# Kernel tuning notes

Measured on AMD Instinct MI355X. Metric: run time of the kernel, lower is better.

The kernel has to match this reference:

```python
import jax, jax.numpy as jnp
import numpy as np

B, S, H = 1, 2048, 4608
NH, NKV, HD = 36, 4, 128
GROUP = NH // NKV  # 9
ROPE_THETA = 100000.0
SLIDING_WINDOW = 1024


def _rope_tables(seq_len, head_dim):
    inv_freq = 1.0 / (ROPE_THETA ** (jnp.arange(0, head_dim, 2, dtype=jnp.float32) / head_dim))
    ang = jnp.arange(seq_len, dtype=jnp.float32)[:, None] * inv_freq[None, :]  # [S, HD/2]
    emb = jnp.concatenate([ang, ang], axis=-1)  # [S, HD]
    return jnp.cos(emb), jnp.sin(emb)


def setup_inputs() -> dict:
    key = jax.random.key(0)
    ks = jax.random.split(key, 10)
    std = 0.02
    cos_table, sin_table = _rope_tables(S, HD)
    return {
        "hidden_states": jax.random.normal(ks[0], (B, S, H), jnp.float32),
        "position_ids": jnp.broadcast_to(jnp.arange(S, dtype=jnp.int64)[None, :], (B, S)),
        "cos_table": cos_table,
        "sin_table": sin_table,
        "q_w": jax.random.normal(ks[1], (NH * HD, H), jnp.float32) * std,
        "q_b": jax.random.normal(ks[2], (NH * HD,), jnp.float32) * std,
        "k_w": jax.random.normal(ks[3], (NKV * HD, H), jnp.float32) * std,
        "k_b": jax.random.normal(ks[4], (NKV * HD,), jnp.float32) * std,
        "v_w": jax.random.normal(ks[5], (NKV * HD, H), jnp.float32) * std,
        "v_b": jax.random.normal(ks[6], (NKV * HD,), jnp.float32) * std,
        "o_w": jax.random.normal(ks[7], (H, NH * HD), jnp.float32) * std,
        "o_b": jax.random.normal(ks[8], (H,), jnp.float32) * std,
        "sliding_window": SLIDING_WINDOW,
    }


def _rotate_half(x):
    x1, x2 = jnp.split(x, 2, axis=-1)
    return jnp.concatenate([-x2, x1], axis=-1)


def reference(hidden_states, position_ids, cos_table, sin_table,
              q_w, q_b, k_w, k_b, v_w, v_b, o_w, o_b, sliding_window):
    bsz, q_len, _ = hidden_states.shape
    scaling = HD ** -0.5

    q = (hidden_states @ q_w.T + q_b).reshape(bsz, q_len, NH, HD)
    k = (hidden_states @ k_w.T + k_b).reshape(bsz, q_len, NKV, HD)
    v = (hidden_states @ v_w.T + v_b).reshape(bsz, q_len, NKV, HD)

    # RoPE with explicit cos/sin, unsqueeze_dim=2 ('bsnd' layout)
    cos = cos_table[position_ids][:, :, None, :]  # [B, S, 1, HD]
    sin = sin_table[position_ids][:, :, None, :]
    q = q * cos + _rotate_half(q) * sin
    k = k * cos + _rotate_half(k) * sin

    # GQA: group Q heads per KV head
    qg = q.reshape(bsz, q_len, NKV, GROUP, HD)
    logits = jnp.einsum('bqgrd,bkgd->bgrqk', qg, k) * scaling  # [B, NKV, GROUP, S, S]

    # causal + sliding-window mask: attend where k <= q and q - k < window
    idx = jnp.arange(q_len)
    mask = (idx[:, None] >= idx[None, :]) & (idx[:, None] - idx[None, :] < sliding_window)
    logits = jnp.where(mask[None, None, None, :, :], logits, jnp.finfo(logits.dtype).min)

    probs = jax.nn.softmax(logits, axis=-1)
    attn = jnp.einsum('bgrqk,bkgd->bqgrd', probs, v).reshape(bsz, q_len, NH * HD)
    return attn @ o_w.T + o_b
```

## Files before the change

kernel.cpp:

```cpp
#include <hip/hip_runtime.h>
#include <stdint.h>

typedef __attribute__((ext_vector_type(8))) __bf16 bf16x8;
typedef __attribute__((ext_vector_type(4))) float f32x4;
typedef __attribute__((ext_vector_type(8))) unsigned short u16x8;
typedef __attribute__((ext_vector_type(4))) unsigned short u16x4;

#define SEQ 2048
#define HID 4608
#define NQKV 5632
#define NHEAD 36
#define NKVH 4
#define HDIM 128
#define WINDOW 1024

__device__ __forceinline__ unsigned short f2b(float f) {
    unsigned u = __builtin_bit_cast(unsigned, f);
    u += 0x7fffu + ((u >> 16) & 1u);
    return (unsigned short)(u >> 16);
}
__device__ __forceinline__ float b2f(unsigned short h) {
    unsigned u = ((unsigned)h) << 16;
    return __builtin_bit_cast(float, u);
}

#define GLD16(gp, lp) __builtin_amdgcn_global_load_lds( \
    (const __attribute__((address_space(1))) void*)(gp), \
    (__attribute__((address_space(3))) void*)(lp), 16, 0, 0)

#define VMCNT8() asm volatile("s_waitcnt vmcnt(8)" ::: "memory")
#define VMCNT4() asm volatile("s_waitcnt vmcnt(4)" ::: "memory")
#define VMCNT0() asm volatile("s_waitcnt vmcnt(0)" ::: "memory")
#define BARRIER() asm volatile("s_barrier" ::: "memory")

__global__ __launch_bounds__(256) void conv_kernel(const float* __restrict__ src,
                                                   unsigned short* __restrict__ dst, int n4) {
    int stride = gridDim.x * blockDim.x;
    for (int i = blockIdx.x * blockDim.x + threadIdx.x; i < n4; i += stride) {
        float4 v = ((const float4*)src)[i];
        ushort4 o;
        o.x = f2b(v.x); o.y = f2b(v.y); o.z = f2b(v.z); o.w = f2b(v.w);
        ((ushort4*)dst)[i] = o;
    }
}

__global__ __launch_bounds__(512, 2) void gemm256_kernel(
    const unsigned short* __restrict__ A,
    const unsigned short* __restrict__ W,
    void* __restrict__ out,
    const float* __restrict__ b0, const float* __restrict__ b1, const float* __restrict__ b2,
    int N, int K, int GX, int outf32)
{
    __shared__ alignas(16) unsigned short ldsA[2][256 * 64];
    __shared__ alignas(16) unsigned short ldsB[2][256 * 64];

    const int tid = threadIdx.x;
    const int w = tid >> 6, lane = tid & 63;
    const int r16 = lane & 15, kg = lane >> 4;
    const int wm = w >> 2, wn = w & 3;

    const int cpx = gridDim.x >> 3;
    const int o = blockIdx.x;
    const int id = (o & 7) * cpx + (o >> 3);
    const int bx = id % GX, by = id / GX;
    const int row0 = by * 256, col0 = bx * 256;

    const int lr = lane >> 3;
    const int lc = lane & 7;
    const int cg = lc ^ lr;
    const unsigned short* Abase = A + (size_t)row0 * K;
    const unsigned short* Wbase = W + (size_t)col0 * K;

    auto STG = [&](const unsigned short* Mat, unsigned short* ldsSlot, int hf, int kb) {
#pragma unroll
        for (int j = 0; j < 2; ++j) {
            int row = hf * 128 + (w * 2 + j) * 8 + lr;
            GLD16(Mat + (size_t)row * K + kb + cg * 8,
                  (char*)ldsSlot + hf * 16384 + (w * 2 + j) * 1024);
        }
    };

    const int NITER = K >> 7;
    f32x4 acc[8][4] = {};
    const int swz = r16 & 7;

    bf16x8 af[4][2], bfA[2][2], bfB[2][2];

#define DSR_A(mh, Sl) \
_Pragma("unroll") for (int mi = 0; mi < 4; ++mi) \
_Pragma("unroll") for (int kh = 0; kh < 2; ++kh) \
    af[mi][kh] = *(const bf16x8*)((Sl) + (wm * 128 + (mh) * 64 + mi * 16 + r16) * 64 + ((kh * 4 + kg) ^ swz) * 8);
#define DSR_B(nh, Sl, BF) \
_Pragma("unroll") for (int ni = 0; ni < 2; ++ni) \
_Pragma("unroll") for (int kh = 0; kh < 2; ++kh) \
    BF[ni][kh] = *(const bf16x8*)((Sl) + (wn * 64 + (nh) * 32 + ni * 16 + r16) * 64 + ((kh * 4 + kg) ^ swz) * 8);
#define MFMA_Q(mh, nh, BF) \
    asm volatile("s_waitcnt lgkmcnt(0)" ::: "memory"); \
    __builtin_amdgcn_sched_barrier(0); \
    __builtin_amdgcn_s_setprio(1); \
_Pragma("unroll") for (int mi = 0; mi < 4; ++mi) \
_Pragma("unroll") for (int ni = 0; ni < 2; ++ni) \
_Pragma("unroll") for (int kh = 0; kh < 2; ++kh) \
    acc[(mh) * 4 + mi][(nh) * 2 + ni] = __builtin_amdgcn_mfma_f32_16x16x32_bf16(af[mi][kh], BF[ni][kh], acc[(mh) * 4 + mi][(nh) * 2 + ni], 0, 0, 0); \
    __builtin_amdgcn_s_setprio(0); \
    __builtin_amdgcn_sched_barrier(0);

    STG(Abase, ldsA[0], 0, 0);  STG(Abase, ldsA[0], 1, 0);
    STG(Wbase, ldsB[0], 0, 0);  STG(Wbase, ldsB[0], 1, 0);
    STG(Abase, ldsA[1], 0, 64); STG(Abase, ldsA[1], 1, 64);
    STG(Wbase, ldsB[1], 0, 64); STG(Wbase, ldsB[1], 1, 64);
    VMCNT0();
    BARRIER();

    for (int i = 0; i < NITER; ++i) {
        const unsigned short* A0 = ldsA[0];
        const unsigned short* B0 = ldsB[0];
        const unsigned short* A1 = ldsA[1];
        const unsigned short* B1 = ldsB[1];
        const bool st = (i + 1 < NITER);
        const int kb0 = (i + 1) * 128;
        const int kb1 = kb0 + 64;

        DSR_A(0, A0); DSR_B(0, B0, bfA);
        BARRIER();
        MFMA_Q(0, 0, bfA);
        BARRIER();
        DSR_B(1, B0, bfB);
        BARRIER();
        MFMA_Q(0, 1, bfB);
        BARRIER();
        DSR_A(1, A0);
        if (st) STG(Wbase, ldsB[0], 0, kb0);
        BARRIER();
        MFMA_Q(1, 1, bfB);
        BARRIER();
        if (st) { STG(Abase, ldsA[0], 0, kb0); VMCNT4(); } else { VMCNT0(); }
        BARRIER();
        MFMA_Q(1, 0, bfA);
        BARRIER();
        DSR_A(0, A1); DSR_B(0, B1, bfA);
        if (st) STG(Abase, ldsA[0], 1, kb0);
        BARRIER();
        MFMA_Q(0, 0, bfA);
        BARRIER();
        DSR_B(1, B1, bfB);
        if (st) STG(Wbase, ldsB[0], 1, kb0);
        BARRIER();
        MFMA_Q(0, 1, bfB);
        BARRIER();
        DSR_A(1, A1);
        if (st) { STG(Wbase, ldsB[1], 0, kb1); STG(Wbase, ldsB[1], 1, kb1); }
        BARRIER();
        MFMA_Q(1, 1, bfB);
        BARRIER();
        if (st) { STG(Abase, ldsA[1], 0, kb1); STG(Abase, ldsA[1], 1, kb1); VMCNT8(); }
        BARRIER();
        MFMA_Q(1, 0, bfA);
        BARRIER();
    }

    if (!outf32) {
        unsigned short* O = (unsigned short*)out;
#pragma unroll
        for (int m = 0; m < 8; ++m)
#pragma unroll
            for (int n = 0; n < 4; ++n)
#pragma unroll
                for (int r = 0; r < 4; ++r) {
                    int row = row0 + wm * 128 + m * 16 + kg * 4 + r;
                    int col = col0 + wn * 64 + n * 16 + r16;
                    float bias = (col < HID) ? b0[col]
                               : (col < HID + 512 ? b1[col - HID] : b2[col - HID - 512]);
                    O[(size_t)row * N + col] = f2b(acc[m][n][r] + bias);
                }
    } else {
        float* O = (float*)out;
#pragma unroll
        for (int m = 0; m < 8; ++m)
#pragma unroll
            for (int n = 0; n < 4; ++n)
#pragma unroll
                for (int r = 0; r < 4; ++r) {
                    int row = row0 + wm * 128 + m * 16 + kg * 4 + r;
                    int col = col0 + wn * 64 + n * 16 + r16;
                    O[(size_t)row * N + col] = acc[m][n][r] + b0[col];
                }
    }
#undef DSR_A
#undef DSR_B
#undef MFMA_Q
}

__global__ __launch_bounds__(256) void rope_kernel(unsigned short* __restrict__ qkv,
                                                   const float* __restrict__ cos_t,
                                                   const float* __restrict__ sin_t) {
    int idx = blockIdx.x * 256 + threadIdx.x;
    int d = idx & 63;
    int t = idx >> 6;
    int head = t % 40;
    int s = t / 40;
    int base = head < NHEAD ? head * HDIM : HID + (head - NHEAD) * HDIM;
    size_t off = (size_t)s * NQKV + base;
    float x = b2f(qkv[off + d]);
    float y = b2f(qkv[off + d + 64]);
    float c = cos_t[s * HDIM + d];
    float sn = sin_t[s * HDIM + d];
    qkv[off + d]      = f2b(x * c - y * sn);
    qkv[off + d + 64] = f2b(y * c + x * sn);
}

__global__ __launch_bounds__(256) void vtrans_kernel(const unsigned short* __restrict__ qkv,
                                                     unsigned short* __restrict__ vtg) {
    __shared__ unsigned short tile[32][36];
    const int s0 = blockIdx.x * 32, d0 = blockIdx.y * 32, kvh = blockIdx.z;
    const int lid = threadIdx.x;
    {
        int sl = lid >> 3, dc = (lid & 7) * 4;
        u16x4 v = *(const u16x4*)(qkv + (size_t)(s0 + sl) * NQKV + HID + 512 + kvh * HDIM + d0 + dc);
#pragma unroll
        for (int i = 0; i < 4; ++i) tile[sl][dc + i] = v[i];
    }
    __syncthreads();
    {
        int dl = lid >> 3, sc = (lid & 7) * 4;
        u16x4 v;
#pragma unroll
        for (int i = 0; i < 4; ++i) v[i] = tile[sc + i][dl];
        *(u16x4*)(vtg + (size_t)kvh * HDIM * SEQ + (size_t)(d0 + dl) * SEQ + s0 + sc) = v;
    }
}

#define KSTR 136
#define VSTR 72
#define PSTR 88
__global__ __launch_bounds__(256) void attn_kernel(const unsigned short* __restrict__ qkv,
                                                   const unsigned short* __restrict__ vtg,
                                                   unsigned short* __restrict__ aout)
{
    __shared__ alignas(16) unsigned short Ks[64 * KSTR];
    __shared__ alignas(16) unsigned short Vt[128 * VSTR];
    __shared__ alignas(16) unsigned short Ps[4 * 16 * PSTR];
    const int h = blockIdx.x, qb = blockIdx.y;
    const int q0 = qb * 64;
    const int kvh = h / 9;
    const int tid = threadIdx.x, wid = tid >> 6, lane = tid & 63;
    const int r16 = lane & 15, kg = lane >> 4;
    const int qbase = q0 + wid * 16;
    const unsigned short* vsrc = vtg + (size_t)kvh * HDIM * SEQ;

    bf16x8 qf[4];
    {
        const unsigned short* qrow = qkv + (size_t)(qbase + r16) * NQKV + h * HDIM;
#pragma unroll
        for (int kk = 0; kk < 4; ++kk)
            qf[kk] = *(const bf16x8*)(qrow + kk * 32 + kg * 8);
    }

    f32x4 o[8] = {};
    float mrow[4], lrow[4];
#pragma unroll
    for (int r = 0; r < 4; ++r) { mrow[r] = -1e30f; lrow[r] = 0.f; }

    int lo = q0 - (WINDOW - 1); if (lo < 0) lo = 0; lo &= ~63;
    unsigned short* myP = Ps + wid * 16 * PSTR;
    const float scale = 0.08838834764831845f;

    for (int kt = lo; kt <= q0; kt += 64) {
        for (int c = tid; c < 1024; c += 256) {
            int key = c >> 4, dc = c & 15;
            const unsigned short* kp = qkv + (size_t)(kt + key) * NQKV + HID + kvh * HDIM + dc * 8;
            *(u16x8*)(Ks + key * KSTR + dc * 8) = *(const u16x8*)kp;
            int d = c >> 3, k8 = (c & 7) * 8;
            *(u16x8*)(Vt + d * VSTR + k8) = *(const u16x8*)(vsrc + (size_t)d * SEQ + kt + k8);
        }
        __syncthreads();

        f32x4 sc[4] = {};
#pragma unroll
        for (int t = 0; t < 4; ++t)
#pragma unroll
            for (int kk = 0; kk < 4; ++kk) {
                bf16x8 kf = *(const bf16x8*)(Ks + (t * 16 + r16) * KSTR + kk * 32 + kg * 8);
                sc[t] = __builtin_amdgcn_mfma_f32_16x16x32_bf16(qf[kk], kf, sc[t], 0, 0, 0);
            }

        float p[4][4], mt[4];
#pragma unroll
        for (int r = 0; r < 4; ++r) mt[r] = -1e30f;
#pragma unroll
        for (int t = 0; t < 4; ++t)
#pragma unroll
            for (int r = 0; r < 4; ++r) {
                int q = qbase + kg * 4 + r;
                int key = kt + t * 16 + r16;
                bool valid = (key <= q) && (q - key < WINDOW);
                float v = valid ? sc[t][r] * scale : -1e30f;
                p[t][r] = v;
                mt[r] = fmaxf(mt[r], v);
            }
#pragma unroll
        for (int mask = 1; mask <= 8; mask <<= 1)
#pragma unroll
            for (int r = 0; r < 4; ++r)
                mt[r] = fmaxf(mt[r], __shfl_xor(mt[r], mask, 64));

        float alpha[4], tsum[4];
#pragma unroll
        for (int r = 0; r < 4; ++r) {
            float mnew = fmaxf(mrow[r], mt[r]);
            alpha[r] = __expf(mrow[r] - mnew);
            mrow[r] = mnew;
            tsum[r] = 0.f;
        }
#pragma unroll
        for (int t = 0; t < 4; ++t)
#pragma unroll
            for (int r = 0; r < 4; ++r) {
                float e = __expf(p[t][r] - mrow[r]);
                p[t][r] = e;
                tsum[r] += e;
            }
#pragma unroll
        for (int mask = 1; mask <= 8; mask <<= 1)
#pragma unroll
            for (int r = 0; r < 4; ++r)
                tsum[r] += __shfl_xor(tsum[r], mask, 64);
#pragma unroll
        for (int r = 0; r < 4; ++r)
            lrow[r] = lrow[r] * alpha[r] + tsum[r];
#pragma unroll
        for (int n = 0; n < 8; ++n)
#pragma unroll
            for (int r = 0; r < 4; ++r)
                o[n][r] = o[n][r] * alpha[r];

#pragma unroll
        for (int t = 0; t < 4; ++t)
#pragma unroll
            for (int r = 0; r < 4; ++r)
                myP[(kg * 4 + r) * PSTR + t * 16 + r16] = f2b(p[t][r]);
        asm volatile("s_waitcnt lgkmcnt(0)" ::: "memory");

#pragma unroll
        for (int kc = 0; kc < 2; ++kc) {
            bf16x8 pa = *(const bf16x8*)(myP + r16 * PSTR + kc * 32 + kg * 8);
#pragma unroll
            for (int n = 0; n < 8; ++n) {
                bf16x8 vb = *(const bf16x8*)(Vt + (n * 16 + r16) * VSTR + kc * 32 + kg * 8);
                o[n] = __builtin_amdgcn_mfma_f32_16x16x32_bf16(pa, vb, o[n], 0, 0, 0);
            }
        }
        __syncthreads();
    }

#pragma unroll
    for (int n = 0; n < 8; ++n)
#pragma unroll
        for (int r = 0; r < 4; ++r) {
            int q = qbase + kg * 4 + r;
            aout[(size_t)q * HID + h * HDIM + n * 16 + r16] = f2b(o[n][r] / lrow[r]);
        }
}

extern "C" void kernel_launch(void* const* d_in, const int* in_sizes, int n_in,
                              void* d_out, int out_size, void* d_ws, size_t ws_size,
                              hipStream_t stream) {
    const float* hidden = (const float*)d_in[0];
    const float* cos_t = (const float*)d_in[2];
    const float* sin_t = (const float*)d_in[3];
    const float* q_w = (const float*)d_in[4];
    const float* q_b = (const float*)d_in[5];
    const float* k_w = (const float*)d_in[6];
    const float* k_b = (const float*)d_in[7];
    const float* v_w = (const float*)d_in[8];
    const float* v_b = (const float*)d_in[9];
    const float* o_w = (const float*)d_in[10];
    const float* o_b = (const float*)d_in[11];

    char* ws = (char*)d_ws;
    unsigned short* hbf  = (unsigned short*)ws;
    unsigned short* attn = hbf;
    unsigned short* wqkv = (unsigned short*)(ws + 18874368);
    unsigned short* vtg  = wqkv;
    unsigned short* wo   = (unsigned short*)(ws + 70778880);
    unsigned short* qkv  = (unsigned short*)(ws + 113246208);

    dim3 blk(256);
    conv_kernel<<<2048, blk, 0, stream>>>(hidden, hbf, (SEQ * HID) / 4);
    conv_kernel<<<2048, blk, 0, stream>>>(q_w, wqkv, (HID * HID) / 4);
    conv_kernel<<<2048, blk, 0, stream>>>(k_w, wqkv + (size_t)HID * HID, (512 * HID) / 4);
    conv_kernel<<<2048, blk, 0, stream>>>(v_w, wqkv + (size_t)5120 * HID, (512 * HID) / 4);
    conv_kernel<<<2048, blk, 0, stream>>>(o_w, wo, (HID * HID) / 4);

    gemm256_kernel<<<dim3(176), dim3(512), 0, stream>>>(hbf, wqkv, qkv, q_b, k_b, v_b, NQKV, HID, 22, 0);
    rope_kernel<<<(SEQ * 40 * 64) / 256, blk, 0, stream>>>(qkv, cos_t, sin_t);
    vtrans_kernel<<<dim3(SEQ / 32, HDIM / 32, NKVH), blk, 0, stream>>>(qkv, vtg);
    attn_kernel<<<dim3(NHEAD, SEQ / 64), blk, 0, stream>>>(qkv, vtg, attn);
    gemm256_kernel<<<dim3(144), dim3(512), 0, stream>>>(attn, wo, d_out, o_b, nullptr, nullptr, HID, HID, 18, 1);
}
```

Measured before the change: 438.8 us.

## Prefetch next K/V tile into registers in attention and merge conversion launches

The attention loop now loads the next 64-key K and V tiles into registers right after the barrier, so the global loads overlap with the QK and PV MFMA work of the current tile. It also replaces the trailing __syncthreads with a raw s_barrier. Separately, the five fp32-to-bf16 conversion launches are merged into one grid-stride kernel that picks source and destination by index range, cutting launch overhead. The prefetch raises register pressure through eight extra 16-byte vectors per thread, which may lower occupancy.

```diff
diff --git a/kernel.cpp b/kernel.cpp
--- a/kernel.cpp
+++ b/kernel.cpp
@@ -33,14 +33,26 @@
 #define VMCNT0() asm volatile("s_waitcnt vmcnt(0)" ::: "memory")
 #define BARRIER() asm volatile("s_barrier" ::: "memory")
 
-__global__ __launch_bounds__(256) void conv_kernel(const float* __restrict__ src,
-                                                   unsigned short* __restrict__ dst, int n4) {
+__global__ __launch_bounds__(256) void conv_all_kernel(
+    const float* __restrict__ s0, unsigned short* __restrict__ d0, int n0,
+    const float* __restrict__ s1, unsigned short* __restrict__ d1, int n1,
+    const float* __restrict__ s2, unsigned short* __restrict__ d2, int n2,
+    const float* __restrict__ s3, unsigned short* __restrict__ d3, int n3,
+    const float* __restrict__ s4, unsigned short* __restrict__ d4, int n4)
+{
+    int total = n0 + n1 + n2 + n3 + n4;
     int stride = gridDim.x * blockDim.x;
-    for (int i = blockIdx.x * blockDim.x + threadIdx.x; i < n4; i += stride) {
-        float4 v = ((const float4*)src)[i];
+    for (int i = blockIdx.x * blockDim.x + threadIdx.x; i < total; i += stride) {
+        const float* src; unsigned short* dst; int j = i;
+        if (j < n0) { src = s0; dst = d0; }
+        else if ((j -= n0) < n1) { src = s1; dst = d1; }
+        else if ((j -= n1) < n2) { src = s2; dst = d2; }
+        else if ((j -= n2) < n3) { src = s3; dst = d3; }
+        else { j -= n3; src = s4; dst = d4; }
+        float4 v = ((const float4*)src)[j];
         ushort4 o;
         o.x = f2b(v.x); o.y = f2b(v.y); o.z = f2b(v.z); o.w = f2b(v.w);
-        ((ushort4*)dst)[i] = o;
+        ((ushort4*)dst)[j] = o;
     }
 }
 
@@ -265,15 +277,30 @@
     unsigned short* myP = Ps + wid * 16 * PSTR;
     const float scale = 0.08838834764831845f;
 
+    u16x8 kreg[4], vreg[4];
+#define PREF(KT) \
+_Pragma("unroll") for (int j = 0; j < 4; ++j) { \
+        int c = tid + j * 256; \
+        int key = c >> 4, dc = c & 15; \
+        kreg[j] = *(const u16x8*)(qkv + (size_t)((KT) + key) * NQKV + HID + kvh * HDIM + dc * 8); \
+        int d = c >> 3, k8 = (c & 7) * 8; \
+        vreg[j] = *(const u16x8*)(vsrc + (size_t)d * SEQ + (KT) + k8); \
+    }
+
+    PREF(lo);
+
     for (int kt = lo; kt <= q0; kt += 64) {
-        for (int c = tid; c < 1024; c += 256) {
+#pragma unroll
+        for (int j = 0; j < 4; ++j) {
+            int c = tid + j * 256;
             int key = c >> 4, dc = c & 15;
-            const unsigned short* kp = qkv + (size_t)(kt + key) * NQKV + HID + kvh * HDIM + dc * 8;
-            *(u16x8*)(Ks + key * KSTR + dc * 8) = *(const u16x8*)kp;
+            *(u16x8*)(Ks + key * KSTR + dc * 8) = kreg[j];
             int d = c >> 3, k8 = (c & 7) * 8;
-            *(u16x8*)(Vt + d * VSTR + k8) = *(const u16x8*)(vsrc + (size_t)d * SEQ + kt + k8);
+            *(u16x8*)(Vt + d * VSTR + k8) = vreg[j];
         }
         __syncthreads();
+
+        if (kt + 64 <= q0) { PREF(kt + 64); }
 
         f32x4 sc[4] = {};
 #pragma unroll
@@ -350,8 +377,9 @@
                 o[n] = __builtin_amdgcn_mfma_f32_16x16x32_bf16(pa, vb, o[n], 0, 0, 0);
             }
         }
-        __syncthreads();
-    }
+        BARRIER();
+    }
+#undef PREF
 
 #pragma unroll
     for (int n = 0; n < 8; ++n)
@@ -386,11 +414,12 @@
     unsigned short* qkv  = (unsigned short*)(ws + 113246208);
 
     dim3 blk(256);
-    conv_kernel<<<2048, blk, 0, stream>>>(hidden, hbf, (SEQ * HID) / 4);
-    conv_kernel<<<2048, blk, 0, stream>>>(q_w, wqkv, (HID * HID) / 4);
-    conv_kernel<<<2048, blk, 0, stream>>>(k_w, wqkv + (size_t)HID * HID, (512 * HID) / 4);
-    conv_kernel<<<2048, blk, 0, stream>>>(v_w, wqkv + (size_t)5120 * HID, (512 * HID) / 4);
-    conv_kernel<<<2048, blk, 0, stream>>>(o_w, wo, (HID * HID) / 4);
+    conv_all_kernel<<<4096, blk, 0, stream>>>(
+        hidden, hbf,                          (SEQ * HID) / 4,
+        q_w,    wqkv,                         (HID * HID) / 4,
+        k_w,    wqkv + (size_t)HID * HID,     (512 * HID) / 4,
+        v_w,    wqkv + (size_t)5120 * HID,    (512 * HID) / 4,
+        o_w,    wo,                           (HID * HID) / 4);
 
     gemm256_kernel<<<dim3(176), dim3(512), 0, stream>>>(hbf, wqkv, qkv, q_b, k_b, v_b, NQKV, HID, 22, 0);
     rope_kernel<<<(SEQ * 40 * 64) / 256, blk, 0, stream>>>(qkv, cos_t, sin_t);
```

Result: no change. 433.0 us (-1.3%).
